# Kernel optimization log

Measured on AMD Instinct MI355X. Metric: run time of the kernel, lower is better.

Reference implementation:

```python
import jax, jax.numpy as jnp
import numpy as np

NUM_HEADS = 8
OUT_FEATS = 128
D_HEAD = OUT_FEATS // NUM_HEADS
N_NODES = 50000
N_EDGES = 600000
IN_FEATS = 128


def setup_inputs() -> dict:
    key = jax.random.key(0)
    ks = jax.random.split(key, 10)
    h = jax.random.normal(ks[0], (N_NODES, IN_FEATS), dtype=jnp.float32)
    src = jax.random.randint(ks[1], (N_EDGES,), 0, N_NODES)
    dst = jax.random.randint(ks[2], (N_EDGES,), 0, N_NODES)
    s = 1.0 / np.sqrt(IN_FEATS)
    W_Q = jax.random.normal(ks[3], (IN_FEATS, OUT_FEATS), dtype=jnp.float32) * s
    W_K = jax.random.normal(ks[4], (IN_FEATS, OUT_FEATS), dtype=jnp.float32) * s
    W_V = jax.random.normal(ks[5], (IN_FEATS, OUT_FEATS), dtype=jnp.float32) * s
    b_Q = jnp.zeros((OUT_FEATS,), dtype=jnp.float32)
    b_K = jnp.zeros((OUT_FEATS,), dtype=jnp.float32)
    b_V = jnp.zeros((OUT_FEATS,), dtype=jnp.float32)
    return {"h": h, "W_Q": W_Q, "b_Q": b_Q, "W_K": W_K, "b_K": b_K,
            "W_V": W_V, "b_V": b_V, "src": src, "dst": dst}


def _graph_conv(h, W, b, src, dst, norm_src, norm_dst):
    # DGL GraphConv, norm='both': D_dst^{-1/2} * A * D_src^{-1/2} * (h W) + b
    x = (h * norm_src[:, None]) @ W                              # [N, F]
    agg = jax.ops.segment_sum(x[src], dst, num_segments=h.shape[0])
    return agg * norm_dst[:, None] + b


def reference(h, W_Q, b_Q, W_K, b_K, W_V, b_V, src, dst):
    N = h.shape[0]
    ones = jnp.ones(src.shape[0], dtype=h.dtype)
    deg_out = jax.ops.segment_sum(ones, src, num_segments=N)   # out-degree (src side)
    deg_in = jax.ops.segment_sum(ones, dst, num_segments=N)    # in-degree (dst side)
    norm_src = jax.lax.rsqrt(jnp.clip(deg_out, 1.0))
    norm_dst = jax.lax.rsqrt(jnp.clip(deg_in, 1.0))

    Q = jax.nn.relu(_graph_conv(h, W_Q, b_Q, src, dst, norm_src, norm_dst))
    K = jax.nn.relu(_graph_conv(h, W_K, b_K, src, dst, norm_src, norm_dst))
    V = jax.nn.relu(_graph_conv(h, W_V, b_V, src, dst, norm_src, norm_dst))

    Qh = Q.reshape(N, NUM_HEADS, D_HEAD)
    Kh = K.reshape(N, NUM_HEADS, D_HEAD)
    Vh = V.reshape(N, NUM_HEADS, D_HEAD)

    # edge-wise scores: K at src dotted with Q at dst, per head
    score = jnp.sum(Kh[src] * Qh[dst], axis=-1, keepdims=True)   # [E, H, 1]
    score = jnp.exp(jnp.clip(score / np.sqrt(D_HEAD), -10.0, 10.0))

    wV = jax.ops.segment_sum(Vh[src] * score, dst, num_segments=N)  # [N, H, Dh]
    z = jax.ops.segment_sum(score, dst, num_segments=N)             # [N, H, 1]
    return wV / (z + 1e-6)
```

## Files before the change

### kernel.cpp

```cpp
#include <hip/hip_runtime.h>

#define INF  128
#define OUTF 128
#define NH   8
#define DHD  16
#define CAP  48

typedef __attribute__((ext_vector_type(8))) short bf16x8;
typedef __attribute__((ext_vector_type(4))) float f32x4;

__device__ __forceinline__ float bf16_to_f32(unsigned short u) {
    union { unsigned int i; float f; } v;
    v.i = ((unsigned int)u) << 16;
    return v.f;
}
__device__ __forceinline__ unsigned short f32_to_bf16(float f) {
    union { float f; unsigned int i; } v;
    v.f = f;
    unsigned int x = v.i;
    return (unsigned short)((x + 0x7fffu + ((x >> 16) & 1u)) >> 16);
}

__global__ void k_front(const int* __restrict__ src, const int* __restrict__ dst,
                        int* __restrict__ deg_out, int* __restrict__ cursor,
                        int* __restrict__ edge_src, int E, int SB, int HB,
                        const float* __restrict__ h, unsigned short* __restrict__ h_b, int N,
                        const float* __restrict__ Wq, const float* __restrict__ Wk,
                        const float* __restrict__ Wv, unsigned short* __restrict__ frag) {
    if (blockIdx.x < (unsigned)SB) {
        int t = blockIdx.x * 256 + threadIdx.x;
        if (t < E) {
            int s = src[t];
            int d = dst[t];
            atomicAdd(&deg_out[s], 1);
            int p = atomicAdd(&cursor[d], 1);
            if (p < CAP) edge_src[d * CAP + p] = s;
        }
    } else if (blockIdx.x < (unsigned)(SB + HB)) {
        int t = (blockIdx.x - SB) * 256 + threadIdx.x;
        if (t < N * (INF / 8)) {
            const float4* p = reinterpret_cast<const float4*>(h + (size_t)t * 8);
            float4 v0 = p[0], v1 = p[1];
            uint4 o;
            o.x = (unsigned int)f32_to_bf16(v0.x) | ((unsigned int)f32_to_bf16(v0.y) << 16);
            o.y = (unsigned int)f32_to_bf16(v0.z) | ((unsigned int)f32_to_bf16(v0.w) << 16);
            o.z = (unsigned int)f32_to_bf16(v1.x) | ((unsigned int)f32_to_bf16(v1.y) << 16);
            o.w = (unsigned int)f32_to_bf16(v1.z) | ((unsigned int)f32_to_bf16(v1.w) << 16);
            *reinterpret_cast<uint4*>(h_b + (size_t)t * 8) = o;
        }
    } else {
        int t = (blockIdx.x - SB - HB) * 256 + threadIdx.x;
        if (t >= 3 * 8 * 4 * 2 * 64) return;
        int lane  = t & 63;
        int plane = (t >> 6) & 1;
        int ks    = (t >> 7) & 3;
        int nt    = (t >> 9) & 7;
        int mat   = t >> 12;
        const float* W = (mat == 0) ? Wq : ((mat == 1) ? Wk : Wv);
        int ln = lane & 15, quad = lane >> 4;
        int n = nt * 16 + ln;
        unsigned short vals[8];
        #pragma unroll
        for (int j = 0; j < 8; ++j) {
            int k = ks * 32 + quad * 8 + j;
            float a = W[k * OUTF + n];
            unsigned short hb = f32_to_bf16(a);
            vals[j] = plane ? f32_to_bf16(a - bf16_to_f32(hb)) : hb;
        }
        unsigned int* dp = reinterpret_cast<unsigned int*>(frag + (size_t)t * 8);
        #pragma unroll
        for (int j = 0; j < 4; ++j)
            dp[j] = (unsigned int)vals[2 * j] | ((unsigned int)vals[2 * j + 1] << 16);
    }
}

__global__ __launch_bounds__(256) void k_agg(const unsigned short* __restrict__ h_b,
                                             const int* __restrict__ deg_out,
                                             const int* __restrict__ cursor,
                                             const int* __restrict__ edge_src,
                                             float* __restrict__ agg, int N) {
    int wid  = (blockIdx.x * 256 + threadIdx.x) >> 6;
    int lane = threadIdx.x & 63;
    if (wid >= N) return;
    int half = lane >> 5, li = lane & 31;
    int c4 = li * 4;
    float a0 = 0.f, a1 = 0.f, a2 = 0.f, a3 = 0.f;
    int deg = cursor[wid]; if (deg > CAP) deg = CAP;
    const int* row = edge_src + wid * CAP;
    auto proc = [&](int e) {
        int s = row[e];
        int dg = deg_out[s]; if (dg < 1) dg = 1;
        float ns = rsqrtf((float)dg);
        uint2 p = *reinterpret_cast<const uint2*>(h_b + (size_t)s * INF + c4);
        a0 += ns * bf16_to_f32((unsigned short)(p.x & 0xffffu));
        a1 += ns * bf16_to_f32((unsigned short)(p.x >> 16));
        a2 += ns * bf16_to_f32((unsigned short)(p.y & 0xffffu));
        a3 += ns * bf16_to_f32((unsigned short)(p.y >> 16));
    };
    int e = half;
    for (; e + 4 <= deg; e += 4) { proc(e); proc(e + 2); }
    for (; e < deg; e += 2) proc(e);
    a0 += __shfl_xor(a0, 32);
    a1 += __shfl_xor(a1, 32);
    a2 += __shfl_xor(a2, 32);
    a3 += __shfl_xor(a3, 32);
    if (half == 0)
        *reinterpret_cast<float4*>(agg + (size_t)wid * INF + c4) =
            make_float4(a0, a1, a2, a3);
}

__global__ __launch_bounds__(256) void k_gemm(const float* __restrict__ agg,
                                              const unsigned short* __restrict__ frag,
                                              const float* __restrict__ bq,
                                              const float* __restrict__ bk,
                                              const float* __restrict__ bv,
                                              const int* __restrict__ cursor,
                                              float* __restrict__ qbuf,
                                              unsigned short* __restrict__ kvbuf,
                                              int N) {
    int mat = blockIdx.y;
    const float* bb = (mat == 0) ? bq : ((mat == 1) ? bk : bv);

    int wave = threadIdx.x >> 6;
    int lane = threadIdx.x & 63;
    int ln   = lane & 15;
    int quad = lane >> 4;
    int mrow = blockIdx.x * 64 + wave * 16;

    bf16x8 ah[4], al[4];
    {
        int m = mrow + ln; if (m >= N) m = N - 1;
        const float* arow = agg + (size_t)m * INF;
        #pragma unroll
        for (int ks = 0; ks < 4; ++ks) {
            const float4* p = reinterpret_cast<const float4*>(arow + ks * 32 + quad * 8);
            float4 v0 = p[0], v1 = p[1];
            float vv[8] = {v0.x, v0.y, v0.z, v0.w, v1.x, v1.y, v1.z, v1.w};
            #pragma unroll
            for (int j = 0; j < 8; ++j) {
                unsigned short hb = f32_to_bf16(vv[j]);
                ah[ks][j] = (short)hb;
                al[ks][j] = (short)f32_to_bf16(vv[j] - bf16_to_f32(hb));
            }
        }
    }

    float nrm[4];
    #pragma unroll
    for (int r = 0; r < 4; ++r) {
        int m = mrow + quad * 4 + r;
        if (m < N) {
            int dg = cursor[m]; if (dg < 1) dg = 1;
            nrm[r] = rsqrtf((float)dg);
        } else nrm[r] = 0.f;
    }

    #pragma unroll 2
    for (int nt = 0; nt < 8; ++nt) {
        int n0 = nt * 16;
        f32x4 acc = {0.f, 0.f, 0.f, 0.f};
        #pragma unroll
        for (int ks = 0; ks < 4; ++ks) {
            size_t base = ((size_t)(((mat * 8 + nt) * 4 + ks) * 2) * 64 + lane) * 8;
            bf16x8 bh = *reinterpret_cast<const bf16x8*>(frag + base);
            bf16x8 bl = *reinterpret_cast<const bf16x8*>(frag + base + 64 * 8);
            acc = __builtin_amdgcn_mfma_f32_16x16x32_bf16(ah[ks], bh, acc, 0, 0, 0);
            acc = __builtin_amdgcn_mfma_f32_16x16x32_bf16(al[ks], bh, acc, 0, 0, 0);
            acc = __builtin_amdgcn_mfma_f32_16x16x32_bf16(ah[ks], bl, acc, 0, 0, 0);
        }
        int col = n0 + ln;
        float bias = bb[col];
        #pragma unroll
        for (int r = 0; r < 4; ++r) {
            int m = mrow + quad * 4 + r;
            if (m < N) {
                float v = acc[r] * nrm[r] + bias;
                v = (v > 0.f) ? v : 0.f;
                if (mat == 0) {
                    qbuf[(size_t)m * OUTF + col] = v;
                } else {
                    int idx = ((col >> 2) << 3) + (col & 3) + ((mat == 2) ? 4 : 0);
                    kvbuf[(size_t)m * 2 * OUTF + idx] = f32_to_bf16(v);
                }
            }
        }
    }
}

__global__ __launch_bounds__(256) void k_attn(const float* __restrict__ qbuf,
                                              const unsigned short* __restrict__ kvbuf,
                                              const int* __restrict__ cursor,
                                              const int* __restrict__ edge_src,
                                              float* __restrict__ out, int N) {
    int wid  = (blockIdx.x * 256 + threadIdx.x) >> 6;
    int lane = threadIdx.x & 63;
    if (wid >= N) return;
    int half = lane >> 5, li = lane & 31;
    int c4 = li * 4;
    float4 q = *reinterpret_cast<const float4*>(qbuf + (size_t)wid * OUTF + c4);
    float a0 = 0.f, a1 = 0.f, a2 = 0.f, a3 = 0.f, z = 0.f;
    int deg = cursor[wid]; if (deg > CAP) deg = CAP;
    const int* row = edge_src + wid * CAP;
    auto proc = [&](int e) {
        int s = row[e];
        uint4 kp = *reinterpret_cast<const uint4*>(kvbuf + (size_t)s * 2 * OUTF + li * 8);
        float p = q.x * bf16_to_f32((unsigned short)(kp.x & 0xffffu))
                + q.y * bf16_to_f32((unsigned short)(kp.x >> 16))
                + q.z * bf16_to_f32((unsigned short)(kp.y & 0xffffu))
                + q.w * bf16_to_f32((unsigned short)(kp.y >> 16));
        p += __shfl_xor(p, 1);
        p += __shfl_xor(p, 2);
        float w = __expf(fminf(fmaxf(0.25f * p, -10.f), 10.f));
        z  += w;
        a0 += w * bf16_to_f32((unsigned short)(kp.z & 0xffffu));
        a1 += w * bf16_to_f32((unsigned short)(kp.z >> 16));
        a2 += w * bf16_to_f32((unsigned short)(kp.w & 0xffffu));
        a3 += w * bf16_to_f32((unsigned short)(kp.w >> 16));
    };
    int e = half;
    for (; e + 4 <= deg; e += 4) { proc(e); proc(e + 2); }
    for (; e < deg; e += 2) proc(e);
    a0 += __shfl_xor(a0, 32);
    a1 += __shfl_xor(a1, 32);
    a2 += __shfl_xor(a2, 32);
    a3 += __shfl_xor(a3, 32);
    z  += __shfl_xor(z, 32);
    if (half == 0) {
        float inv = 1.0f / (z + 1e-6f);
        *reinterpret_cast<float4*>(out + (size_t)wid * OUTF + c4) =
            make_float4(a0 * inv, a1 * inv, a2 * inv, a3 * inv);
    }
}

extern "C" void kernel_launch(void* const* d_in, const int* in_sizes, int n_in,
                              void* d_out, int out_size, void* d_ws, size_t ws_size,
                              hipStream_t stream) {
    const float* h  = (const float*)d_in[0];
    const float* Wq = (const float*)d_in[1];
    const float* bq = (const float*)d_in[2];
    const float* Wk = (const float*)d_in[3];
    const float* bk = (const float*)d_in[4];
    const float* Wv = (const float*)d_in[5];
    const float* bv = (const float*)d_in[6];
    const int* src = (const int*)d_in[7];
    const int* dst = (const int*)d_in[8];

    const int N = in_sizes[0] / INF;
    const int E = in_sizes[7];

    char* ws = (char*)d_ws;
    size_t off = 0;
    auto carve = [&](size_t bytes) -> void* {
        void* p = ws + off;
        off = (off + bytes + 255) & ~(size_t)255;
        return p;
    };
    int*   zeroed    = (int*)  carve((size_t)2 * N * sizeof(int));
    int*   deg_out   = zeroed;
    int*   cursor    = zeroed + N;
    int*   edge_src  = (int*)  carve((size_t)N * CAP * sizeof(int));
    unsigned short* h_b  = (unsigned short*)carve((size_t)N * INF * sizeof(unsigned short));
    float* agg       = (float*)carve((size_t)N * INF * sizeof(float));
    float* qbuf      = (float*)carve((size_t)N * OUTF * sizeof(float));
    unsigned short* kvbuf = (unsigned short*)carve((size_t)N * 2 * OUTF * sizeof(unsigned short));
    unsigned short* wfrag = (unsigned short*)carve((size_t)3 * 8 * 4 * 2 * 64 * 8 * sizeof(unsigned short));
    (void)ws_size;

    float* out = (float*)d_out;

    hipMemsetAsync(zeroed, 0, (size_t)2 * N * sizeof(int), stream);

    int SB = (E + 255) / 256;
    int HB = (N * (INF / 8) + 255) / 256;
    int WB = (3 * 8 * 4 * 2 * 64 + 255) / 256;
    k_front<<<SB + HB + WB, 256, 0, stream>>>(src, dst, deg_out, cursor, edge_src,
                                              E, SB, HB, h, h_b, N, Wq, Wk, Wv, wfrag);

    int gAgg = (N + 3) / 4;
    k_agg<<<gAgg, 256, 0, stream>>>(h_b, deg_out, cursor, edge_src, agg, N);

    dim3 gemm_grid((N + 63) / 64, 3);
    k_gemm<<<gemm_grid, 256, 0, stream>>>(agg, wfrag, bq, bk, bv,
                                          cursor, qbuf, kvbuf, N);

    k_attn<<<gAgg, 256, 0, stream>>>(qbuf, kvbuf, cursor, edge_src, out, N);
}
```

Baseline: 272.0 us.

## Fuse neighbor aggregation into the QKV GEMM kernel via LDS tile

Merges the aggregation and GEMM kernels: each wave aggregates 16 destination nodes sequentially into a padded shared-memory tile, then runs the MFMA projection for all three matrices from that tile. This removes the fp32 agg buffer's global write and three re-reads plus one launch. In exchange, each wave now processes 16 nodes serially rather than one node per wave, so parallelism for latency-bound gathers drops about 16x, and LDS use per block rises.

```diff
diff --git a/kernel.cpp b/kernel.cpp
--- a/kernel.cpp
+++ b/kernel.cpp
@@ -5,6 +5,7 @@
 #define NH   8
 #define DHD  16
 #define CAP  48
+#define TPAD 132
 
 typedef __attribute__((ext_vector_type(8))) short bf16x8;
 typedef __attribute__((ext_vector_type(4))) float f32x4;
@@ -74,66 +75,60 @@
     }
 }
 
-__global__ __launch_bounds__(256) void k_agg(const unsigned short* __restrict__ h_b,
-                                             const int* __restrict__ deg_out,
-                                             const int* __restrict__ cursor,
-                                             const int* __restrict__ edge_src,
-                                             float* __restrict__ agg, int N) {
-    int wid  = (blockIdx.x * 256 + threadIdx.x) >> 6;
-    int lane = threadIdx.x & 63;
-    if (wid >= N) return;
-    int half = lane >> 5, li = lane & 31;
-    int c4 = li * 4;
-    float a0 = 0.f, a1 = 0.f, a2 = 0.f, a3 = 0.f;
-    int deg = cursor[wid]; if (deg > CAP) deg = CAP;
-    const int* row = edge_src + wid * CAP;
-    auto proc = [&](int e) {
-        int s = row[e];
-        int dg = deg_out[s]; if (dg < 1) dg = 1;
-        float ns = rsqrtf((float)dg);
-        uint2 p = *reinterpret_cast<const uint2*>(h_b + (size_t)s * INF + c4);
-        a0 += ns * bf16_to_f32((unsigned short)(p.x & 0xffffu));
-        a1 += ns * bf16_to_f32((unsigned short)(p.x >> 16));
-        a2 += ns * bf16_to_f32((unsigned short)(p.y & 0xffffu));
-        a3 += ns * bf16_to_f32((unsigned short)(p.y >> 16));
-    };
-    int e = half;
-    for (; e + 4 <= deg; e += 4) { proc(e); proc(e + 2); }
-    for (; e < deg; e += 2) proc(e);
-    a0 += __shfl_xor(a0, 32);
-    a1 += __shfl_xor(a1, 32);
-    a2 += __shfl_xor(a2, 32);
-    a3 += __shfl_xor(a3, 32);
-    if (half == 0)
-        *reinterpret_cast<float4*>(agg + (size_t)wid * INF + c4) =
-            make_float4(a0, a1, a2, a3);
-}
-
-__global__ __launch_bounds__(256) void k_gemm(const float* __restrict__ agg,
-                                              const unsigned short* __restrict__ frag,
-                                              const float* __restrict__ bq,
-                                              const float* __restrict__ bk,
-                                              const float* __restrict__ bv,
-                                              const int* __restrict__ cursor,
-                                              float* __restrict__ qbuf,
-                                              unsigned short* __restrict__ kvbuf,
-                                              int N) {
-    int mat = blockIdx.y;
-    const float* bb = (mat == 0) ? bq : ((mat == 1) ? bk : bv);
-
+__global__ __launch_bounds__(256) void k_aggemm(const unsigned short* __restrict__ h_b,
+                                                const int* __restrict__ deg_out,
+                                                const int* __restrict__ cursor,
+                                                const int* __restrict__ edge_src,
+                                                const unsigned short* __restrict__ frag,
+                                                const float* __restrict__ bq,
+                                                const float* __restrict__ bk,
+                                                const float* __restrict__ bv,
+                                                float* __restrict__ qbuf,
+                                                unsigned short* __restrict__ kvbuf,
+                                                int N) {
+    __shared__ float tile[4][16][TPAD];
     int wave = threadIdx.x >> 6;
     int lane = threadIdx.x & 63;
+    int half = lane >> 5, li = lane & 31;
+    int c4   = li * 4;
+    int mrow = blockIdx.x * 64 + wave * 16;
+
+    for (int r = 0; r < 16; ++r) {
+        int node = mrow + r;
+        float a0 = 0.f, a1 = 0.f, a2 = 0.f, a3 = 0.f;
+        if (node < N) {
+            int deg = cursor[node]; if (deg > CAP) deg = CAP;
+            const int* rowp = edge_src + node * CAP;
+            auto proc = [&](int e) {
+                int s = rowp[e];
+                int dg = deg_out[s]; if (dg < 1) dg = 1;
+                float ns = rsqrtf((float)dg);
+                uint2 p = *reinterpret_cast<const uint2*>(h_b + (size_t)s * INF + c4);
+                a0 += ns * bf16_to_f32((unsigned short)(p.x & 0xffffu));
+                a1 += ns * bf16_to_f32((unsigned short)(p.x >> 16));
+                a2 += ns * bf16_to_f32((unsigned short)(p.y & 0xffffu));
+                a3 += ns * bf16_to_f32((unsigned short)(p.y >> 16));
+            };
+            int e = half;
+            for (; e + 4 <= deg; e += 4) { proc(e); proc(e + 2); }
+            for (; e < deg; e += 2) proc(e);
+        }
+        a0 += __shfl_xor(a0, 32);
+        a1 += __shfl_xor(a1, 32);
+        a2 += __shfl_xor(a2, 32);
+        a3 += __shfl_xor(a3, 32);
+        if (half == 0)
+            *reinterpret_cast<float4*>(&tile[wave][r][c4]) = make_float4(a0, a1, a2, a3);
+    }
+
     int ln   = lane & 15;
     int quad = lane >> 4;
-    int mrow = blockIdx.x * 64 + wave * 16;
-
     bf16x8 ah[4], al[4];
     {
-        int m = mrow + ln; if (m >= N) m = N - 1;
-        const float* arow = agg + (size_t)m * INF;
+        const float* trow = &tile[wave][ln][0];
         #pragma unroll
         for (int ks = 0; ks < 4; ++ks) {
-            const float4* p = reinterpret_cast<const float4*>(arow + ks * 32 + quad * 8);
+            const float4* p = reinterpret_cast<const float4*>(trow + ks * 32 + quad * 8);
             float4 v0 = p[0], v1 = p[1];
             float vv[8] = {v0.x, v0.y, v0.z, v0.w, v1.x, v1.y, v1.z, v1.w};
             #pragma unroll
@@ -155,32 +150,35 @@
         } else nrm[r] = 0.f;
     }
 
-    #pragma unroll 2
-    for (int nt = 0; nt < 8; ++nt) {
-        int n0 = nt * 16;
-        f32x4 acc = {0.f, 0.f, 0.f, 0.f};
-        #pragma unroll
-        for (int ks = 0; ks < 4; ++ks) {
-            size_t base = ((size_t)(((mat * 8 + nt) * 4 + ks) * 2) * 64 + lane) * 8;
-            bf16x8 bh = *reinterpret_cast<const bf16x8*>(frag + base);
-            bf16x8 bl = *reinterpret_cast<const bf16x8*>(frag + base + 64 * 8);
-            acc = __builtin_amdgcn_mfma_f32_16x16x32_bf16(ah[ks], bh, acc, 0, 0, 0);
-            acc = __builtin_amdgcn_mfma_f32_16x16x32_bf16(al[ks], bh, acc, 0, 0, 0);
-            acc = __builtin_amdgcn_mfma_f32_16x16x32_bf16(ah[ks], bl, acc, 0, 0, 0);
-        }
-        int col = n0 + ln;
-        float bias = bb[col];
-        #pragma unroll
-        for (int r = 0; r < 4; ++r) {
-            int m = mrow + quad * 4 + r;
-            if (m < N) {
-                float v = acc[r] * nrm[r] + bias;
-                v = (v > 0.f) ? v : 0.f;
-                if (mat == 0) {
-                    qbuf[(size_t)m * OUTF + col] = v;
-                } else {
-                    int idx = ((col >> 2) << 3) + (col & 3) + ((mat == 2) ? 4 : 0);
-                    kvbuf[(size_t)m * 2 * OUTF + idx] = f32_to_bf16(v);
+    #pragma unroll
+    for (int mat = 0; mat < 3; ++mat) {
+        const float* bb = (mat == 0) ? bq : ((mat == 1) ? bk : bv);
+        #pragma unroll 2
+        for (int nt = 0; nt < 8; ++nt) {
+            f32x4 acc = {0.f, 0.f, 0.f, 0.f};
+            #pragma unroll
+            for (int ks = 0; ks < 4; ++ks) {
+                size_t base = ((size_t)(((mat * 8 + nt) * 4 + ks) * 2) * 64 + lane) * 8;
+                bf16x8 bh = *reinterpret_cast<const bf16x8*>(frag + base);
+                bf16x8 bl = *reinterpret_cast<const bf16x8*>(frag + base + 64 * 8);
+                acc = __builtin_amdgcn_mfma_f32_16x16x32_bf16(ah[ks], bh, acc, 0, 0, 0);
+                acc = __builtin_amdgcn_mfma_f32_16x16x32_bf16(al[ks], bh, acc, 0, 0, 0);
+                acc = __builtin_amdgcn_mfma_f32_16x16x32_bf16(ah[ks], bl, acc, 0, 0, 0);
+            }
+            int col = nt * 16 + ln;
+            float bias = bb[col];
+            #pragma unroll
+            for (int r = 0; r < 4; ++r) {
+                int m = mrow + quad * 4 + r;
+                if (m < N) {
+                    float v = acc[r] * nrm[r] + bias;
+                    v = (v > 0.f) ? v : 0.f;
+                    if (mat == 0) {
+                        qbuf[(size_t)m * OUTF + col] = v;
+                    } else {
+                        int idx = ((col >> 2) << 3) + (col & 3) + ((mat == 2) ? 4 : 0);
+                        kvbuf[(size_t)m * 2 * OUTF + idx] = f32_to_bf16(v);
+                    }
                 }
             }
         }
@@ -260,7 +258,6 @@
     int*   cursor    = zeroed + N;
     int*   edge_src  = (int*)  carve((size_t)N * CAP * sizeof(int));
     unsigned short* h_b  = (unsigned short*)carve((size_t)N * INF * sizeof(unsigned short));
-    float* agg       = (float*)carve((size_t)N * INF * sizeof(float));
     float* qbuf      = (float*)carve((size_t)N * OUTF * sizeof(float));
     unsigned short* kvbuf = (unsigned short*)carve((size_t)N * 2 * OUTF * sizeof(unsigned short));
     unsigned short* wfrag = (unsigned short*)carve((size_t)3 * 8 * 4 * 2 * 64 * 8 * sizeof(unsigned short));
@@ -276,12 +273,10 @@
     k_front<<<SB + HB + WB, 256, 0, stream>>>(src, dst, deg_out, cursor, edge_src,
                                               E, SB, HB, h, h_b, N, Wq, Wk, Wv, wfrag);
 
-    int gAgg = (N + 3) / 4;
-    k_agg<<<gAgg, 256, 0, stream>>>(h_b, deg_out, cursor, edge_src, agg, N);
-
-    dim3 gemm_grid((N + 63) / 64, 3);
-    k_gemm<<<gemm_grid, 256, 0, stream>>>(agg, wfrag, bq, bk, bv,
-                                          cursor, qbuf, kvbuf, N);
-
-    k_attn<<<gAgg, 256, 0, stream>>>(qbuf, kvbuf, cursor, edge_src, out, N);
-}
+    int gFuse = (N + 63) / 64;
+    k_aggemm<<<gFuse, 256, 0, stream>>>(h_b, deg_out, cursor, edge_src, wfrag,
+                                        bq, bk, bv, qbuf, kvbuf, N);
+
+    int gAttn = (N + 3) / 4;
+    k_attn<<<gAttn, 256, 0, stream>>>(qbuf, kvbuf, cursor, edge_src, out, N);
+}
```

Result: slower. 282.4 us (+3.8%).
